# Performance work log

Hardware: AMD Instinct MI355X
Metric: run time of the kernel (lower is better)

Reference implementation:

```python
import jax, jax.numpy as jnp
import numpy as np
import math

FS, N_FFT, NUM_BANDS, NUM_BINS = 16000, 512, 31, 257
H = 96  # dim_hidden

def band_partition():
    f_min, f_max = FS / N_FFT, FS / 2.0
    z_min = 69.0 + 12.0 * math.log2(f_min / 440.0)
    z_max = 69.0 + 12.0 * math.log2(f_max / 440.0)
    z = np.linspace(z_min, z_max, NUM_BANDS + 2)
    f_points = 440.0 * 2.0 ** ((z - 69.0) / 12.0)
    bins = np.round(f_points * N_FFT / FS).astype(np.int64)
    bins[0] = 0
    bands = []
    for i in range(NUM_BANDS):
        s = max(0, int(bins[i]))
        e = min(NUM_BINS, int(bins[i + 2]) + 1)
        if e <= s:
            e = s + 1
        bands.append((s, e))
    return bands

BANDS = band_partition()

def hann(L):
    # torch.hann_window default (periodic=True)
    return 0.5 - 0.5 * jnp.cos(2.0 * jnp.pi * jnp.arange(L, dtype=jnp.float32) / L)

def chan_ln(x, eps=1e-5):
    # AdaNorm2d assumed = LayerNorm over channel dim, no affine
    m = jnp.mean(x, axis=1, keepdims=True)
    v = jnp.var(x, axis=1, keepdims=True)
    return (x - m) * jax.lax.rsqrt(v + eps)

def prelu(x, a):
    return jnp.where(x >= 0, x, a * x)

def setup_inputs() -> dict:
    key = jax.random.key(0)
    ks = jax.random.split(key, 20)
    B, T = 4, 1000
    return {
        'mix_repr': jax.random.normal(ks[0], (B, H, NUM_BINS, T), jnp.float32),
        'spin': jax.random.normal(ks[1], (B, 64, NUM_BINS, T), jnp.float32),
        'doa': jax.random.normal(ks[2], (B, 36), jnp.float32),
        'enc_w': jax.random.normal(ks[3], (NUM_BANDS, H, 64), jnp.float32) * 0.05,
        'enc_b': jax.random.normal(ks[4], (NUM_BANDS, H), jnp.float32) * 0.05,
        'enc_a': 0.25 * jnp.ones((NUM_BANDS,), jnp.float32),
        'dqg_w': jax.random.normal(ks[5], (NUM_BANDS, 2 * H, 36), jnp.float32) * 0.05,
        'dqg_b': jax.random.normal(ks[6], (NUM_BANDS, 2 * H), jnp.float32) * 0.05,
        'dec_w': jax.random.normal(ks[7], (NUM_BANDS, H, H), jnp.float32) * 0.05,
        'dec_b': jax.random.normal(ks[8], (NUM_BANDS, H), jnp.float32) * 0.05,
        'dec_a': 0.25 * jnp.ones((NUM_BANDS,), jnp.float32),
        'qw': jax.random.normal(ks[9], (H, H), jnp.float32) * 0.05,
        'qb': jax.random.normal(ks[10], (H,), jnp.float32) * 0.05,
        'kw': jax.random.normal(ks[11], (H, H), jnp.float32) * 0.05,
        'kb': jax.random.normal(ks[12], (H,), jnp.float32) * 0.05,
        'vw': jax.random.normal(ks[13], (H, H), jnp.float32) * 0.05,
        'vb': jax.random.normal(ks[14], (H,), jnp.float32) * 0.05,
        'ow': jax.random.normal(ks[15], (H, H), jnp.float32) * 0.05,
        'ob': jax.random.normal(ks[16], (H,), jnp.float32) * 0.05,
    }

def reference(mix_repr, spin, doa, enc_w, enc_b, enc_a, dqg_w, dqg_b,
              dec_w, dec_b, dec_a, qw, qb, kw, kb, vw, vb, ow, ob):
    B, D, F, T = mix_repr.shape
    merged = jnp.zeros((B, H, F, T), mix_repr.dtype)
    wsum = jnp.zeros((F,), mix_repr.dtype)
    for k, (s, e) in enumerate(BANDS):  # fixed set of 31 static ragged bands
        L = e - s
        win = hann(L)
        sub = spin[:, :, s:e, :]                                   # [B,64,L,T]
        feat = jnp.einsum('oc,bcft->boft', enc_w[k], sub) + enc_b[k][None, :, None, None]
        feat = prelu(chan_ln(feat), enc_a[k])
        qp = doa @ dqg_w[k].T + dqg_b[k]                           # [B,2H]
        gamma, beta = qp[:, :H], qp[:, H:]
        tgt = (1.0 + gamma)[:, :, None, None] * feat + beta[:, :, None, None]
        dec = jnp.einsum('oc,bcft->boft', dec_w[k], tgt) + dec_b[k][None, :, None, None]
        dec = prelu(chan_ln(dec), dec_a[k])
        merged = merged.at[:, :, s:e, :].add(dec * win[None, None, :, None])
        wsum = wsum.at[s:e].add(win)
    merged = merged / jnp.clip(wsum, 1e-8)[None, None, :, None]
    # MixtureQueryFusion: 1x1 conv cross-attention gate
    Q = jnp.einsum('oc,bcft->boft', qw, mix_repr) + qb[None, :, None, None]
    K = jnp.einsum('oc,bcft->boft', kw, merged) + kb[None, :, None, None]
    V = jnp.einsum('oc,bcft->boft', vw, merged) + vb[None, :, None, None]
    attn = jax.nn.sigmoid(jnp.sum(Q * K, axis=1, keepdims=True) / jnp.sqrt(jnp.float32(H)))
    attended = V * attn
    out = mix_repr + jnp.einsum('oc,bcft->boft', ow, attended) + ob[None, :, None, None]
    return out
```

## Files before the change

### kernel.cpp

```cpp
#include <hip/hip_runtime.h>
#include <math.h>

#define NBANDS 31
#define FT 257000

typedef __attribute__((ext_vector_type(8))) short bh8;
typedef __attribute__((ext_vector_type(4))) float f4;

__constant__ int d_bs[NBANDS] = {0,1,1,2,2,2,3,3,4,5,6,7,8,10,11,13,16,19,23,27,32,38,45,54,64,76,91,108,128,152,181};
__constant__ int d_be[NBANDS] = {2,3,3,3,4,4,5,6,7,8,9,11,12,14,17,20,24,28,33,39,46,55,65,77,92,109,129,153,182,216,257};

__device__ __forceinline__ unsigned short b16u(float v) {
  __bf16 h = (__bf16)v;
  return __builtin_bit_cast(unsigned short, h);
}
__device__ __forceinline__ unsigned pk2(float a, float b) {
  return (unsigned)b16u(a) | ((unsigned)b16u(b) << 16);
}
__device__ __forceinline__ float hann1(int i, int L) {
  return 0.5f - 0.5f * cosf(6.283185307179586f * (float)i / (float)L);
}

__global__ __launch_bounds__(256) void prep_w(
    const float* __restrict__ enc_w, const float* __restrict__ dec_w,
    const float* __restrict__ qw, const float* __restrict__ kw,
    const float* __restrict__ vw, const float* __restrict__ ow,
    unsigned short* __restrict__ w16) {
  const int stride = gridDim.x * blockDim.x;
  for (int i = blockIdx.x * blockDim.x + threadIdx.x; i < 513024; i += stride) {
    float v;
    if (i < 190464) {
      const int k = i / 6144, r = i - k * 6144;
      const int tile = r >> 9, li = r & 511;
      const int lane = li >> 3, j = li & 7;
      const int g = lane >> 4, n = lane & 15;
      const int mt = tile >> 1, kt = tile & 1;
      v = enc_w[k * 6144 + (mt * 16 + n) * 64 + kt * 32 + g * 8 + j];
    } else if (i < 476160) {
      const int i2 = i - 190464;
      const int k = i2 / 9216, r = i2 - k * 9216;
      const int tile = r >> 9, li = r & 511;
      const int lane = li >> 3, j = li & 7;
      const int g = lane >> 4, n = lane & 15;
      const int mt = tile / 3, kt = tile - mt * 3;
      v = dec_w[k * 9216 + (mt * 16 + n) * 96 + kt * 32 + g * 8 + j];
    } else {
      const int i2 = i - 476160;
      const int a = i2 / 9216, r = i2 - a * 9216;
      const int tile = r >> 9, li = r & 511;
      const int lane = li >> 3, j = li & 7;
      const int g = lane >> 4, n = lane & 15;
      const int mt = tile / 3, kt = tile - mt * 3;
      const float* src = (a == 0) ? qw : (a == 1) ? kw : (a == 2) ? vw : ow;
      v = src[(mt * 16 + n) * 96 + kt * 32 + g * 8 + j];
    }
    w16[i] = b16u(v);
  }
}

__global__ __launch_bounds__(192) void qp_kernel(const float* __restrict__ doa,
                                                 const float* __restrict__ dqg_w,
                                                 const float* __restrict__ dqg_b,
                                                 float* __restrict__ gbuf) {
  const int k = blockIdx.x, b = blockIdx.y;
  const int tid = threadIdx.x;
  __shared__ float sdoa[36];
  if (tid < 36) sdoa[tid] = doa[b * 36 + tid];
  __syncthreads();
  const float* wr = dqg_w + (k * 192 + tid) * 36;
  float acc = dqg_b[k * 192 + tid];
  #pragma unroll
  for (int i = 0; i < 36; ++i) acc = fmaf(wr[i], sdoa[i], acc);
  if (tid < 96) acc += 1.0f;
  gbuf[(k * 4 + b) * 192 + tid] = acc;
}

__global__ __launch_bounds__(320) void tab_kernel(float* __restrict__ ftab) {
  const int f = blockIdx.x * blockDim.x + threadIdx.x;
  if (f >= 257) return;
  int k0 = 0; while (d_be[k0] <= f) ++k0;
  int k1 = k0; while (k1 < NBANDS && d_bs[k1] <= f) ++k1;
  float wsum = 0.f, wn[5];
  for (int k = k0; k < k1; ++k) {
    const float wv = hann1(f - d_bs[k], d_be[k] - d_bs[k]);
    wn[k - k0] = wv; wsum += wv;
  }
  float* o = ftab + f * 8;
  o[0] = (float)k0; o[1] = (float)(k1 - k0); o[2] = 1.0f / fmaxf(wsum, 1e-8f);
  #pragma unroll
  for (int j = 0; j < 5; ++j) o[3 + j] = (j < k1 - k0) ? wn[j] : 0.f;
}

#define LDSWAIT asm volatile("s_waitcnt lgkmcnt(0)" ::: "memory")

__device__ __forceinline__ void init6(f4* acc, const float* s, int off) {
  #pragma unroll
  for (int mt = 0; mt < 6; ++mt) {
    const float4 bb = *reinterpret_cast<const float4*>(s + mt * 16 + off);
    acc[mt] = (f4){bb.x, bb.y, bb.z, bb.w};
  }
}
__device__ __forceinline__ void ln96(const f4* acc, float& mean, float& rs) {
  float sm = 0.f, sq = 0.f;
  #pragma unroll
  for (int mt = 0; mt < 6; ++mt)
    #pragma unroll
    for (int r = 0; r < 4; ++r) { const float v = acc[mt][r]; sm += v; sq = fmaf(v, v, sq); }
  sm += __shfl_xor(sm, 16); sm += __shfl_xor(sm, 32);
  sq += __shfl_xor(sq, 16); sq += __shfl_xor(sq, 32);
  mean = sm * (1.f / 96.f);
  rs = rsqrtf(sq * (1.f / 96.f) - mean * mean + 1e-5f);
}
__device__ __forceinline__ void load6s(bh8* dst, const unsigned short* p, int step9) {
  #pragma unroll
  for (int mt = 0; mt < 6; ++mt)
    dst[mt] = *reinterpret_cast<const bh8*>(p + ((mt * step9) << 9));
}

__global__ __launch_bounds__(256, 3) void fused_mfma(
    const float* __restrict__ mix, const float* __restrict__ spin,
    const unsigned short* __restrict__ enc16, const float* __restrict__ enc_b, const float* __restrict__ enc_a,
    const unsigned short* __restrict__ dec16, const float* __restrict__ dec_b, const float* __restrict__ dec_a,
    const float* __restrict__ gb, const float* __restrict__ ftab,
    const unsigned short* __restrict__ q16, const float* __restrict__ qb,
    const unsigned short* __restrict__ k16, const float* __restrict__ kb,
    const unsigned short* __restrict__ v16, const float* __restrict__ vb,
    const unsigned short* __restrict__ o16, const float* __restrict__ ob,
    float* __restrict__ out) {
  const int id0 = (int)blockIdx.x;
  const int id  = (id0 & 7) * 2056 + (id0 >> 3);
  const int tt  = id & 15;
  const int fb  = id >> 4;
  const int f   = fb % 257;
  const int b   = fb / 257;
  const int t0  = tt << 6;

  const int tid  = threadIdx.x;
  const int lane = tid & 63;
  const int w    = tid >> 6;
  const int g    = lane >> 4;
  const int n    = lane & 15;
  const int col  = (w << 4) + n;
  const int t    = t0 + col;
  const bool tv  = t < 1000;
  const int tcl  = tv ? t : 999;
  const int sw   = (n & 7) << 3;
  const int lb   = lane << 3;

  __shared__ __align__(16) unsigned short XT[64 * 128];
  __shared__ __align__(16) float stage[5 * 512 + 384];
  unsigned short* xw = XT + col * 128;

  const float* ft = ftab + f * 8;
  const int k0 = (int)ft[0];
  const int nb = (int)ft[1];
  const float winv = ft[2];

  {
    const int tot = (nb << 9) + 384;
    for (int i = tid; i < tot; i += 256) {
      const int kk = i >> 9, r = i & 511;
      float v = 0.f;
      if (kk < nb) {
        const int k = k0 + kk;
        if      (r < 96)  v = enc_b[k * 96 + r];
        else if (r < 192) v = dec_b[k * 96 + (r - 96)];
        else if (r < 384) v = gb[(k * 4 + b) * 192 + (r - 192)];
        else if (r == 384) v = enc_a[k];
        else if (r == 385) v = dec_a[k];
        else if (r == 386) v = ft[3 + kk];
      } else {
        const int r2 = i - (nb << 9);
        v = (r2 < 96) ? qb[r2] : (r2 < 192) ? kb[r2 - 96] : (r2 < 288) ? vb[r2 - 192] : ob[r2 - 288];
      }
      stage[i] = v;
    }
  }

  const float* spL = spin + b * 64 * FT + f * 1000 + tcl;
  const float* mxL = mix  + b * 96 * FT + f * 1000 + tcl;

  bh8 spb[2];
  {
    float spf[16];
    #pragma unroll
    for (int j = 0; j < 8; ++j) spf[j]     = __builtin_nontemporal_load(spL + (g * 8 + j) * FT);
    #pragma unroll
    for (int j = 0; j < 8; ++j) spf[8 + j] = __builtin_nontemporal_load(spL + (32 + g * 8 + j) * FT);
    #pragma unroll
    for (int kt = 0; kt < 2; ++kt)
      #pragma unroll
      for (int j = 0; j < 8; ++j) spb[kt][j] = (short)b16u(spf[kt * 8 + j]);
  }

  bh8 pre[6];
  load6s(pre, enc16 + k0 * 6144 + lb, 2);

  __syncthreads();

  f4 macc[6];
  #pragma unroll
  for (int mt = 0; mt < 6; ++mt) macc[mt] = (f4){0.f, 0.f, 0.f, 0.f};

  const int oo = g * 4;

  for (int kk = 0; kk < nb; ++kk) {
    const int k = k0 + kk;
    const unsigned short* ew  = enc16 + k * 6144 + lb;
    const unsigned short* dwp = dec16 + k * 9216 + lb;
    const float* stg = stage + (kk << 9);

    f4 acc[6];
    init6(acc, stg, oo);
    #pragma unroll
    for (int mt = 0; mt < 6; ++mt)
      acc[mt] = __builtin_amdgcn_mfma_f32_16x16x32_bf16(pre[mt], spb[0], acc[mt], 0, 0, 0);
    #pragma unroll
    for (int mt = 0; mt < 6; ++mt) {
      const bh8 af = *reinterpret_cast<const bh8*>(ew + ((mt * 2 + 1) << 9));
      acc[mt] = __builtin_amdgcn_mfma_f32_16x16x32_bf16(af, spb[1], acc[mt], 0, 0, 0);
    }

    load6s(pre, dwp, 3);

    float mean, rs;
    ln96(acc, mean, rs);
    const float ea = stg[384];
    #pragma unroll
    for (int mt = 0; mt < 6; ++mt) {
      const float4 ga = *reinterpret_cast<const float4*>(stg + 192 + mt * 16 + oo);
      const float4 be = *reinterpret_cast<const float4*>(stg + 288 + mt * 16 + oo);
      float x0 = (acc[mt][0] - mean) * rs; x0 = (x0 >= 0.f) ? x0 : ea * x0;
      float x1 = (acc[mt][1] - mean) * rs; x1 = (x1 >= 0.f) ? x1 : ea * x1;
      float x2 = (acc[mt][2] - mean) * rs; x2 = (x2 >= 0.f) ? x2 : ea * x2;
      float x3 = (acc[mt][3] - mean) * rs; x3 = (x3 >= 0.f) ? x3 : ea * x3;
      uint2 u;
      u.x = pk2(fmaf(ga.x, x0, be.x), fmaf(ga.y, x1, be.y));
      u.y = pk2(fmaf(ga.z, x2, be.z), fmaf(ga.w, x3, be.w));
      *reinterpret_cast<uint2*>(xw + ((mt * 16 + g * 4) ^ sw)) = u;
    }
    LDSWAIT;

    f4 dacc[6];
    init6(dacc, stg + 96, oo);
    {
      const bh8 bf0 = *reinterpret_cast<const bh8*>(xw + ((0 * 32 + g * 8) ^ sw));
      #pragma unroll
      for (int mt = 0; mt < 6; ++mt)
        dacc[mt] = __builtin_amdgcn_mfma_f32_16x16x32_bf16(pre[mt], bf0, dacc[mt], 0, 0, 0);
    }

    {
      const bool more = (kk + 1 < nb);
      load6s(pre, more ? (enc16 + (k + 1) * 6144 + lb) : (q16 + lb), more ? 2 : 3);
    }

    #pragma unroll
    for (int kt = 1; kt < 3; ++kt) {
      const bh8 bf = *reinterpret_cast<const bh8*>(xw + ((kt * 32 + g * 8) ^ sw));
      #pragma unroll
      for (int mt = 0; mt < 6; ++mt) {
        const bh8 af = *reinterpret_cast<const bh8*>(dwp + ((mt * 3 + kt) << 9));
        dacc[mt] = __builtin_amdgcn_mfma_f32_16x16x32_bf16(af, bf, dacc[mt], 0, 0, 0);
      }
    }
    float mean2, rs2;
    ln96(dacc, mean2, rs2);
    const float da = stg[385];
    const float win = stg[386];
    #pragma unroll
    for (int mt = 0; mt < 6; ++mt)
      #pragma unroll
      for (int r = 0; r < 4; ++r) {
        float x = (dacc[mt][r] - mean2) * rs2;
        x = (x >= 0.f) ? x : da * x;
        macc[mt][r] = fmaf(win, x, macc[mt][r]);
      }
  }

  float mxf[24];
  #pragma unroll
  for (int kt = 0; kt < 3; ++kt)
    #pragma unroll
    for (int j = 0; j < 8; ++j) mxf[kt * 8 + j] = mxL[(kt * 32 + g * 8 + j) * FT];

  #pragma unroll
  for (int mt = 0; mt < 6; ++mt) {
    uint2 u;
    u.x = pk2(macc[mt][0] * winv, macc[mt][1] * winv);
    u.y = pk2(macc[mt][2] * winv, macc[mt][3] * winv);
    *reinterpret_cast<uint2*>(xw + ((mt * 16 + g * 4) ^ sw)) = u;
  }
  LDSWAIT;
  bh8 gfr[3];
  #pragma unroll
  for (int kt = 0; kt < 3; ++kt) gfr[kt] = *reinterpret_cast<const bh8*>(xw + ((kt * 32 + g * 8) ^ sw));

  bh8 mxb[3];
  #pragma unroll
  for (int kt = 0; kt < 3; ++kt)
    #pragma unroll
    for (int j = 0; j < 8; ++j) mxb[kt][j] = (short)b16u(mxf[kt * 8 + j]);

  const float* stQ = stage + (nb << 9);

  f4 qacc[6];
  init6(qacc, stQ, oo);
  const unsigned short* qp16 = q16 + lb;
  #pragma unroll
  for (int mt = 0; mt < 6; ++mt)
    qacc[mt] = __builtin_amdgcn_mfma_f32_16x16x32_bf16(pre[mt], mxb[0], qacc[mt], 0, 0, 0);
  load6s(pre, k16 + lb, 3);
  #pragma unroll
  for (int kt = 1; kt < 3; ++kt)
    #pragma unroll
    for (int mt = 0; mt < 6; ++mt) {
      const bh8 af = *reinterpret_cast<const bh8*>(qp16 + ((mt * 3 + kt) << 9));
      qacc[mt] = __builtin_amdgcn_mfma_f32_16x16x32_bf16(af, mxb[kt], qacc[mt], 0, 0, 0);
    }
  f4 kacc[6];
  init6(kacc, stQ + 96, oo);
  const unsigned short* kp16 = k16 + lb;
  #pragma unroll
  for (int mt = 0; mt < 6; ++mt)
    kacc[mt] = __builtin_amdgcn_mfma_f32_16x16x32_bf16(pre[mt], gfr[0], kacc[mt], 0, 0, 0);
  load6s(pre, v16 + lb, 3);
  #pragma unroll
  for (int kt = 1; kt < 3; ++kt)
    #pragma unroll
    for (int mt = 0; mt < 6; ++mt) {
      const bh8 af = *reinterpret_cast<const bh8*>(kp16 + ((mt * 3 + kt) << 9));
      kacc[mt] = __builtin_amdgcn_mfma_f32_16x16x32_bf16(af, gfr[kt], kacc[mt], 0, 0, 0);
    }
  float p = 0.f;
  #pragma unroll
  for (int mt = 0; mt < 6; ++mt)
    #pragma unroll
    for (int r = 0; r < 4; ++r) p = fmaf(qacc[mt][r], kacc[mt][r], p);
  p += __shfl_xor(p, 16); p += __shfl_xor(p, 32);
  const float sig = 1.f / (1.f + __expf(-p * 0.10206207261596575f));

  f4 vacc[6];
  init6(vacc, stQ + 192, oo);
  const unsigned short* vp16 = v16 + lb;
  #pragma unroll
  for (int mt = 0; mt < 6; ++mt)
    vacc[mt] = __builtin_amdgcn_mfma_f32_16x16x32_bf16(pre[mt], gfr[0], vacc[mt], 0, 0, 0);
  load6s(pre, o16 + lb, 3);
  #pragma unroll
  for (int kt = 1; kt < 3; ++kt)
    #pragma unroll
    for (int mt = 0; mt < 6; ++mt) {
      const bh8 af = *reinterpret_cast<const bh8*>(vp16 + ((mt * 3 + kt) << 9));
      vacc[mt] = __builtin_amdgcn_mfma_f32_16x16x32_bf16(af, gfr[kt], vacc[mt], 0, 0, 0);
    }
  #pragma unroll
  for (int mt = 0; mt < 6; ++mt) {
    uint2 u;
    u.x = pk2(vacc[mt][0] * sig, vacc[mt][1] * sig);
    u.y = pk2(vacc[mt][2] * sig, vacc[mt][3] * sig);
    *reinterpret_cast<uint2*>(xw + ((mt * 16 + g * 4) ^ sw)) = u;
  }
  float mres[6][4];
  #pragma unroll
  for (int mt = 0; mt < 6; ++mt)
    #pragma unroll
    for (int r = 0; r < 4; ++r) mres[mt][r] = mxL[(mt * 16 + g * 4 + r) * FT];
  LDSWAIT;
  bh8 afr[3];
  #pragma unroll
  for (int kt = 0; kt < 3; ++kt) afr[kt] = *reinterpret_cast<const bh8*>(xw + ((kt * 32 + g * 8) ^ sw));

  f4 oacc[6];
  init6(oacc, stQ + 288, oo);
  const unsigned short* op16 = o16 + lb;
  #pragma unroll
  for (int mt = 0; mt < 6; ++mt)
    oacc[mt] = __builtin_amdgcn_mfma_f32_16x16x32_bf16(pre[mt], afr[0], oacc[mt], 0, 0, 0);
  #pragma unroll
  for (int kt = 1; kt < 3; ++kt)
    #pragma unroll
    for (int mt = 0; mt < 6; ++mt) {
      const bh8 af = *reinterpret_cast<const bh8*>(op16 + ((mt * 3 + kt) << 9));
      oacc[mt] = __builtin_amdgcn_mfma_f32_16x16x32_bf16(af, afr[kt], oacc[mt], 0, 0, 0);
    }

  if (tv) {
    #pragma unroll
    for (int mt = 0; mt < 6; ++mt) {
      const int base = (b * 96 + mt * 16 + g * 4) * FT + f * 1000 + t;
      #pragma unroll
      for (int r = 0; r < 4; ++r)
        __builtin_nontemporal_store(mres[mt][r] + oacc[mt][r], out + base + r * FT);
    }
  }
}

extern "C" void kernel_launch(void* const* d_in, const int* in_sizes, int n_in,
                              void* d_out, int out_size, void* d_ws, size_t ws_size,
                              hipStream_t stream) {
  (void)in_sizes; (void)n_in; (void)out_size; (void)ws_size;
  const float* mix   = (const float*)d_in[0];
  const float* spin  = (const float*)d_in[1];
  const float* doa   = (const float*)d_in[2];
  const float* enc_w = (const float*)d_in[3];
  const float* enc_b = (const float*)d_in[4];
  const float* enc_a = (const float*)d_in[5];
  const float* dqg_w = (const float*)d_in[6];
  const float* dqg_b = (const float*)d_in[7];
  const float* dec_w = (const float*)d_in[8];
  const float* dec_b = (const float*)d_in[9];
  const float* dec_a = (const float*)d_in[10];
  const float* qw    = (const float*)d_in[11];
  const float* qb    = (const float*)d_in[12];
  const float* kw    = (const float*)d_in[13];
  const float* kb    = (const float*)d_in[14];
  const float* vw    = (const float*)d_in[15];
  const float* vb    = (const float*)d_in[16];
  const float* oww   = (const float*)d_in[17];
  const float* obb   = (const float*)d_in[18];
  float* outp = (float*)d_out;

  unsigned short* w16 = (unsigned short*)d_ws;
  unsigned short* enc16 = w16;
  unsigned short* dec16 = w16 + 190464;
  unsigned short* q16   = w16 + 476160;
  unsigned short* k16   = q16 + 9216;
  unsigned short* v16   = k16 + 9216;
  unsigned short* o16   = v16 + 9216;
  float* gbws = (float*)((char*)d_ws + 1026048);
  float* ftab = (float*)((char*)d_ws + 1121280);

  hipLaunchKernelGGL(prep_w, dim3(512), dim3(256), 0, stream,
                     enc_w, dec_w, qw, kw, vw, oww, w16);
  hipLaunchKernelGGL(qp_kernel, dim3(NBANDS, 4), dim3(192), 0, stream,
                     doa, dqg_w, dqg_b, gbws);
  hipLaunchKernelGGL(tab_kernel, dim3(1), dim3(320), 0, stream, ftab);
  hipLaunchKernelGGL(fused_mfma, dim3(16448), dim3(256), 0, stream,
                     mix, spin, enc16, enc_b, enc_a, dec16, dec_b, dec_a, gbws, ftab,
                     q16, qb, k16, kb, v16, vb, o16, obb, outp);
}
```

Baseline: 583.3 us.

## Restructure attention GEMMs per output tile to cut registers and raise occupancy

After: 671.8 us. +15.2%, slower.

```diff
diff --git a/kernel.cpp b/kernel.cpp
--- a/kernel.cpp
+++ b/kernel.cpp
@@ -100,6 +100,10 @@
     acc[mt] = (f4){bb.x, bb.y, bb.z, bb.w};
   }
 }
+__device__ __forceinline__ f4 init1(const float* s, int mt, int off) {
+  const float4 bb = *reinterpret_cast<const float4*>(s + mt * 16 + off);
+  return (f4){bb.x, bb.y, bb.z, bb.w};
+}
 __device__ __forceinline__ void ln96(const f4* acc, float& mean, float& rs) {
   float sm = 0.f, sq = 0.f;
   #pragma unroll
@@ -117,7 +121,7 @@
     dst[mt] = *reinterpret_cast<const bh8*>(p + ((mt * step9) << 9));
 }
 
-__global__ __launch_bounds__(256, 3) void fused_mfma(
+__global__ __launch_bounds__(256, 4) void fused_mfma(
     const float* __restrict__ mix, const float* __restrict__ spin,
     const unsigned short* __restrict__ enc16, const float* __restrict__ enc_b, const float* __restrict__ enc_a,
     const unsigned short* __restrict__ dec16, const float* __restrict__ dec_b, const float* __restrict__ dec_a,
@@ -278,11 +282,18 @@
       }
   }
 
-  float mxf[24];
-  #pragma unroll
-  for (int kt = 0; kt < 3; ++kt)
-    #pragma unroll
-    for (int j = 0; j < 8; ++j) mxf[kt * 8 + j] = mxL[(kt * 32 + g * 8 + j) * FT];
+  bh8 mxb[3];
+  {
+    float mxf[24];
+    #pragma unroll
+    for (int kt = 0; kt < 3; ++kt)
+      #pragma unroll
+      for (int j = 0; j < 8; ++j) mxf[kt * 8 + j] = mxL[(kt * 32 + g * 8 + j) * FT];
+    #pragma unroll
+    for (int kt = 0; kt < 3; ++kt)
+      #pragma unroll
+      for (int j = 0; j < 8; ++j) mxb[kt][j] = (short)b16u(mxf[kt * 8 + j]);
+  }
 
   #pragma unroll
   for (int mt = 0; mt < 6; ++mt) {
@@ -296,69 +307,45 @@
   #pragma unroll
   for (int kt = 0; kt < 3; ++kt) gfr[kt] = *reinterpret_cast<const bh8*>(xw + ((kt * 32 + g * 8) ^ sw));
 
-  bh8 mxb[3];
-  #pragma unroll
-  for (int kt = 0; kt < 3; ++kt)
-    #pragma unroll
-    for (int j = 0; j < 8; ++j) mxb[kt][j] = (short)b16u(mxf[kt * 8 + j]);
-
   const float* stQ = stage + (nb << 9);
-
-  f4 qacc[6];
-  init6(qacc, stQ, oo);
   const unsigned short* qp16 = q16 + lb;
-  #pragma unroll
-  for (int mt = 0; mt < 6; ++mt)
-    qacc[mt] = __builtin_amdgcn_mfma_f32_16x16x32_bf16(pre[mt], mxb[0], qacc[mt], 0, 0, 0);
-  load6s(pre, k16 + lb, 3);
-  #pragma unroll
-  for (int kt = 1; kt < 3; ++kt)
-    #pragma unroll
-    for (int mt = 0; mt < 6; ++mt) {
+  const unsigned short* kp16 = k16 + lb;
+  const unsigned short* vp16 = v16 + lb;
+  const unsigned short* op16 = o16 + lb;
+
+  float p = 0.f;
+  #pragma unroll
+  for (int mt = 0; mt < 6; ++mt) {
+    f4 qa = init1(stQ, mt, oo);
+    qa = __builtin_amdgcn_mfma_f32_16x16x32_bf16(pre[mt], mxb[0], qa, 0, 0, 0);
+    #pragma unroll
+    for (int kt = 1; kt < 3; ++kt) {
       const bh8 af = *reinterpret_cast<const bh8*>(qp16 + ((mt * 3 + kt) << 9));
-      qacc[mt] = __builtin_amdgcn_mfma_f32_16x16x32_bf16(af, mxb[kt], qacc[mt], 0, 0, 0);
-    }
-  f4 kacc[6];
-  init6(kacc, stQ + 96, oo);
-  const unsigned short* kp16 = k16 + lb;
-  #pragma unroll
-  for (int mt = 0; mt < 6; ++mt)
-    kacc[mt] = __builtin_amdgcn_mfma_f32_16x16x32_bf16(pre[mt], gfr[0], kacc[mt], 0, 0, 0);
-  load6s(pre, v16 + lb, 3);
-  #pragma unroll
-  for (int kt = 1; kt < 3; ++kt)
-    #pragma unroll
-    for (int mt = 0; mt < 6; ++mt) {
+      qa = __builtin_amdgcn_mfma_f32_16x16x32_bf16(af, mxb[kt], qa, 0, 0, 0);
+    }
+    f4 ka = init1(stQ + 96, mt, oo);
+    #pragma unroll
+    for (int kt = 0; kt < 3; ++kt) {
       const bh8 af = *reinterpret_cast<const bh8*>(kp16 + ((mt * 3 + kt) << 9));
-      kacc[mt] = __builtin_amdgcn_mfma_f32_16x16x32_bf16(af, gfr[kt], kacc[mt], 0, 0, 0);
-    }
-  float p = 0.f;
-  #pragma unroll
-  for (int mt = 0; mt < 6; ++mt)
-    #pragma unroll
-    for (int r = 0; r < 4; ++r) p = fmaf(qacc[mt][r], kacc[mt][r], p);
+      ka = __builtin_amdgcn_mfma_f32_16x16x32_bf16(af, gfr[kt], ka, 0, 0, 0);
+    }
+    #pragma unroll
+    for (int r = 0; r < 4; ++r) p = fmaf(qa[r], ka[r], p);
+  }
   p += __shfl_xor(p, 16); p += __shfl_xor(p, 32);
   const float sig = 1.f / (1.f + __expf(-p * 0.10206207261596575f));
 
-  f4 vacc[6];
-  init6(vacc, stQ + 192, oo);
-  const unsigned short* vp16 = v16 + lb;
-  #pragma unroll
-  for (int mt = 0; mt < 6; ++mt)
-    vacc[mt] = __builtin_amdgcn_mfma_f32_16x16x32_bf16(pre[mt], gfr[0], vacc[mt], 0, 0, 0);
-  load6s(pre, o16 + lb, 3);
-  #pragma unroll
-  for (int kt = 1; kt < 3; ++kt)
-    #pragma unroll
-    for (int mt = 0; mt < 6; ++mt) {
+  #pragma unroll
+  for (int mt = 0; mt < 6; ++mt) {
+    f4 va = init1(stQ + 192, mt, oo);
+    #pragma unroll
+    for (int kt = 0; kt < 3; ++kt) {
       const bh8 af = *reinterpret_cast<const bh8*>(vp16 + ((mt * 3 + kt) << 9));
-      vacc[mt] = __builtin_amdgcn_mfma_f32_16x16x32_bf16(af, gfr[kt], vacc[mt], 0, 0, 0);
-    }
-  #pragma unroll
-  for (int mt = 0; mt < 6; ++mt) {
+      va = __builtin_amdgcn_mfma_f32_16x16x32_bf16(af, gfr[kt], va, 0, 0, 0);
+    }
     uint2 u;
-    u.x = pk2(vacc[mt][0] * sig, vacc[mt][1] * sig);
-    u.y = pk2(vacc[mt][2] * sig, vacc[mt][3] * sig);
+    u.x = pk2(va[0] * sig, va[1] * sig);
+    u.y = pk2(va[2] * sig, va[3] * sig);
     *reinterpret_cast<uint2*>(xw + ((mt * 16 + g * 4) ^ sw)) = u;
   }
   float mres[6][4];
@@ -371,27 +358,19 @@
   #pragma unroll
   for (int kt = 0; kt < 3; ++kt) afr[kt] = *reinterpret_cast<const bh8*>(xw + ((kt * 32 + g * 8) ^ sw));
 
-  f4 oacc[6];
-  init6(oacc, stQ + 288, oo);
-  const unsigned short* op16 = o16 + lb;
-  #pragma unroll
-  for (int mt = 0; mt < 6; ++mt)
-    oacc[mt] = __builtin_amdgcn_mfma_f32_16x16x32_bf16(pre[mt], afr[0], oacc[mt], 0, 0, 0);
-  #pragma unroll
-  for (int kt = 1; kt < 3; ++kt)
-    #pragma unroll
-    for (int mt = 0; mt < 6; ++mt) {
+  #pragma unroll
+  for (int mt = 0; mt < 6; ++mt) {
+    f4 oa = init1(stQ + 288, mt, oo);
+    #pragma unroll
+    for (int kt = 0; kt < 3; ++kt) {
       const bh8 af = *reinterpret_cast<const bh8*>(op16 + ((mt * 3 + kt) << 9));
-      oacc[mt] = __builtin_amdgcn_mfma_f32_16x16x32_bf16(af, afr[kt], oacc[mt], 0, 0, 0);
-    }
-
-  if (tv) {
-    #pragma unroll
-    for (int mt = 0; mt < 6; ++mt) {
+      oa = __builtin_amdgcn_mfma_f32_16x16x32_bf16(af, afr[kt], oa, 0, 0, 0);
+    }
+    if (tv) {
       const int base = (b * 96 + mt * 16 + g * 4) * FT + f * 1000 + t;
       #pragma unroll
       for (int r = 0; r < 4; ++r)
-        __builtin_nontemporal_store(mres[mt][r] + oacc[mt][r], out + base + r * FT);
+        __builtin_nontemporal_store(mres[mt][r] + oa[r], out + base + r * FT);
     }
   }
 }
```
